# Kernel tuning notes

Hardware: AMD Instinct MI355X
Metric: run time of the kernel (lower is better)

Reference implementation:

```python
import jax, jax.numpy as jnp
import numpy as np

N = 100000
E = 1600000
IN_CH = 128
OUT_CH = 128
NUM_REL = 16
NUM_BASES = 8


def setup_inputs() -> dict:
    key = jax.random.key(0)
    k1, k2, k3, k4, k5, k6 = jax.random.split(key, 6)
    x = jax.random.normal(k1, (N, IN_CH), dtype=jnp.float32)
    edge_index = jax.random.randint(k2, (2, E), 0, N, dtype=jnp.int64)
    edge_type = jax.random.randint(k3, (E,), 0, NUM_REL, dtype=jnp.int64)
    # glorot-style init for basis weights (last slot = root weight) and comp
    wscale = np.sqrt(6.0 / (IN_CH + OUT_CH)).astype(np.float32)
    weight = jax.random.uniform(k4, (NUM_BASES + 1, IN_CH, OUT_CH), dtype=jnp.float32,
                                minval=-wscale, maxval=wscale)
    cscale = np.sqrt(6.0 / (NUM_REL + NUM_BASES)).astype(np.float32)
    comp = jax.random.uniform(k5, (NUM_REL, NUM_BASES), dtype=jnp.float32,
                              minval=-cscale, maxval=cscale)
    bias = jnp.zeros((OUT_CH,), dtype=jnp.float32)
    return {"x": x, "weight": weight, "comp": comp, "bias": bias,
            "edge_index": edge_index, "edge_type": edge_type, "num_nodes": N}


def reference(x, weight, comp, bias, edge_index, edge_type, num_nodes):
    """RGCN with basis decomposition, mean aggregation, root weight + bias.

    agg[i, b, :] = (1/deg(i)) * sum_{e: dst(e)=i} comp[etype(e), b] * x[src(e)]
    out = concat_b(agg, x_root) @ weight.reshape(-1, out_ch) + bias
    """
    src = edge_index[0]
    dst = edge_index[1]
    num_bases = comp.shape[1]
    coeff = comp[edge_type]            # [E, B] per-edge basis coefficients
    msg = x[src]                       # [E, in] gathered neighbor features
    # per-basis scatter-add into destination nodes (loop over small fixed B)
    aggs = [jax.ops.segment_sum(msg * coeff[:, b:b + 1], dst, num_segments=num_nodes)
            for b in range(num_bases)]
    agg = jnp.stack(aggs, axis=1)      # [N, B, in]
    # mean normalization by in-degree of destination node
    deg = jax.ops.segment_sum(jnp.ones((src.shape[0],), dtype=x.dtype), dst,
                              num_segments=num_nodes)
    agg = agg / jnp.maximum(deg, 1.0)[:, None, None]
    # [N, (B+1)*in]: bases first, then root features (matches weight layout)
    feat = jnp.concatenate([agg.reshape(num_nodes, -1), x], axis=1)
    out = feat @ weight.reshape(-1, weight.shape[-1]) + bias
    return out
```

## Files before the change

### kernel.cpp

```cpp
#include <hip/hip_runtime.h>
#include <hip/hip_bf16.h>
#include <stdint.h>


#define FPAD 1160
#define SCAT_CH 8192

typedef __attribute__((ext_vector_type(8))) __bf16 bf16x8;
typedef __attribute__((ext_vector_type(4))) float f32x4;
typedef __attribute__((ext_vector_type(2))) float f32x2;

#define RFL(v) __builtin_amdgcn_readfirstlane(v)

__global__ __launch_bounds__(256) void k_prep(const float* __restrict__ x,
                                              __hip_bfloat16* __restrict__ xb,
                                              uint8_t* __restrict__ xq, int n4,
                                              const float* __restrict__ W,
                                              __hip_bfloat16* __restrict__ Wf,
                                              const int* __restrict__ dst, int E,
                                              int* __restrict__ bcnt, int NB,
                                              int xbB, int wpB, int hbB) {
    extern __shared__ int sc[];
    int b = blockIdx.x;
    if (b < xbB) {
        int i = b * 256 + threadIdx.x;
        if (i < n4) {
            float4 v = ((const float4*)x)[i];
            __hip_bfloat16 h0 = __float2bfloat16(v.x), h1 = __float2bfloat16(v.y);
            __hip_bfloat16 h2 = __float2bfloat16(v.z), h3 = __float2bfloat16(v.w);
            uint32_t p0 = ((uint32_t)*(uint16_t*)&h1 << 16) | *(uint16_t*)&h0;
            uint32_t p1 = ((uint32_t)*(uint16_t*)&h3 << 16) | *(uint16_t*)&h2;
            ((uint2*)xb)[i] = make_uint2(p0, p1);
            uint32_t q = __builtin_amdgcn_cvt_pk_fp8_f32(v.x, v.y, 0u, 0);
            q = __builtin_amdgcn_cvt_pk_fp8_f32(v.z, v.w, q, 1);
            ((uint32_t*)xq)[i] = q;
        }
    } else if (b < xbB + wpB) {
        int idx = (b - xbB) * 256 + threadIdx.x;
        if (idx < 1152 * 128) {
            int k = idx >> 7, n = idx & 127;
            int kb = k >> 5, hi = (k >> 3) & 3, j = k & 7;
            Wf[((((kb << 2) + hi) << 7 | n) << 3) | j] = __float2bfloat16(W[idx]);
        }
    } else {
        for (int i = threadIdx.x; i < NB; i += 256) sc[i] = 0;
        __syncthreads();
        int hb = b - xbB - wpB;
        int stride = hbB * 256;
        for (int e = hb * 256 + threadIdx.x; e < E; e += stride)
            atomicAdd(&sc[dst[e] >> 7], 1);
        __syncthreads();
        for (int i = threadIdx.x; i < NB; i += 256) {
            int c = sc[i];
            if (c) atomicAdd(&bcnt[i], c);
        }
    }
}

__global__ __launch_bounds__(1024) void k_bscan(const int* __restrict__ bcnt, int NB,
                                                int E, int N,
                                                int* __restrict__ base,
                                                int* __restrict__ cursor,
                                                int* __restrict__ row_ptr,
                                                int* __restrict__ csr) {
    __shared__ int s[1024];
    int t = threadIdx.x;
    int v = (t < NB) ? bcnt[t] : 0;
    s[t] = v;
    __syncthreads();
    for (int off = 1; off < 1024; off <<= 1) {
        int u = (t >= off) ? s[t - off] : 0;
        __syncthreads();
        s[t] += u;
        __syncthreads();
    }
    int excl = (t > 0) ? s[t - 1] : 0;
    if (t < NB) { base[t] = excl; cursor[t] = excl; }
    if (t == 0) { base[NB] = E; row_ptr[N] = E; }
    if (t < 24) csr[E + t] = 0;
}

__global__ __launch_bounds__(256) void k_bscatter(const int* __restrict__ src,
                                                  const int* __restrict__ dst,
                                                  const int* __restrict__ et,
                                                  int E, int NB,
                                                  int* __restrict__ cursor,
                                                  int* __restrict__ brec) {
    extern __shared__ int sm[];
    int* cnt = sm;
    int* gb  = sm + NB;
    for (int i = threadIdx.x; i < NB; i += 256) cnt[i] = 0;
    __syncthreads();
    int e0 = blockIdx.x * SCAT_CH;
    int e1 = min(e0 + SCAT_CH, E);
    for (int e = e0 + threadIdx.x; e < e1; e += 256)
        atomicAdd(&cnt[dst[e] >> 7], 1);
    __syncthreads();
    for (int i = threadIdx.x; i < NB; i += 256) {
        int c = cnt[i];
        gb[i] = c ? atomicAdd(&cursor[i], c) : 0;
    }
    __syncthreads();
    for (int i = threadIdx.x; i < NB; i += 256) cnt[i] = 0;
    __syncthreads();
    for (int e = e0 + threadIdx.x; e < e1; e += 256) {
        int d = dst[e];
        int bk = d >> 7;
        int off = atomicAdd(&cnt[bk], 1);
        brec[gb[bk] + off] = (src[e] << 11) | ((d & 127) << 4) | (et[e] & 15);
    }
}

__global__ __launch_bounds__(256) void k_bsort(const int* __restrict__ brec,
                                               const int* __restrict__ base,
                                               int N,
                                               int* __restrict__ row_ptr,
                                               int* __restrict__ csr) {
    __shared__ int cnt[128], st[128];
    int b = blockIdx.x;
    int s0 = base[b], s1 = base[b + 1];
    int t = threadIdx.x;
    if (t < 128) cnt[t] = 0;
    __syncthreads();
    for (int i = s0 + t; i < s1; i += 256)
        atomicAdd(&cnt[(brec[i] >> 4) & 127], 1);
    __syncthreads();
    if (t < 128) st[t] = cnt[t];
    __syncthreads();
    for (int off = 1; off < 128; off <<= 1) {
        int u = 0;
        if (t < 128 && t >= off) u = st[t - off];
        __syncthreads();
        if (t < 128) st[t] += u;
        __syncthreads();
    }
    if (t < 128) {
        int excl = st[t] - cnt[t];
        int d = b * 128 + t;
        if (d < N) row_ptr[d] = s0 + excl;
        cnt[t] = excl;
    }
    __syncthreads();
    for (int i = s0 + t; i < s1; i += 256) {
        int r = brec[i];
        int d7 = (r >> 4) & 127;
        int off = atomicAdd(&cnt[d7], 1);
        csr[s0 + off] = ((r >> 11) << 4) | (r & 15);
    }
}

#define GATH(pp) ((uint32_t)xq16[(uint32_t)((pp) >> 4) * 64u + (uint32_t)lane])

#define CONS1(pp, raw) do {                                               \
    uint32_t _r = (raw);                                                  \
    float _x0 = __builtin_amdgcn_cvt_f32_fp8(_r, 0);                      \
    float _x1 = __builtin_amdgcn_cvt_f32_fp8(_r, 1);                      \
    const f32x2* _cf = (const f32x2*)(comp + ((pp) & 15) * 8);            \
    f32x2 _xx0 = (f32x2){_x0, _x0};                                       \
    f32x2 _xx1 = (f32x2){_x1, _x1};                                       \
    f32x2 _c0 = _cf[0], _c1 = _cf[1], _c2 = _cf[2], _c3 = _cf[3];         \
    a0[0] += _c0 * _xx0; a0[1] += _c1 * _xx0;                             \
    a0[2] += _c2 * _xx0; a0[3] += _c3 * _xx0;                             \
    a1[0] += _c0 * _xx1; a1[1] += _c1 * _xx1;                             \
    a1[2] += _c2 * _xx1; a1[3] += _c3 * _xx1;                             \
} while (0)

__global__ __launch_bounds__(512, 8) void k_fused(const uint8_t* __restrict__ xq,
                                                  const __hip_bfloat16* __restrict__ xb,
                                                  const float* __restrict__ comp,
                                                  const int* __restrict__ row_ptr,
                                                  const int* __restrict__ csr,
                                                  const __hip_bfloat16* __restrict__ Wf,
                                                  const float* __restrict__ bias,
                                                  float* __restrict__ out, int M) {
    __shared__ __hip_bfloat16 fl[16][FPAD];
    __shared__ int snext;
    const uint16_t* __restrict__ xq16 = (const uint16_t*)xq;
    const uint32_t* __restrict__ xb32 = (const uint32_t*)xb;
    int t = threadIdx.x;
    int wid = t >> 6, lane = t & 63;
    int i0 = blockIdx.x * 16;
    if (t == 0) snext = 0;
    __syncthreads();

    #pragma unroll 1
    while (true) {
        int grab = 0;
        if (lane == 0) grab = atomicAdd(&snext, 1);
        int lr = RFL(__shfl(grab, 0));
        if (lr >= 16) break;
        int iu = i0 + lr;
        f32x2 a0[4], a1[4];
        #pragma unroll
        for (int b = 0; b < 4; b++) { a0[b] = (f32x2){0.f, 0.f}; a1[b] = (f32x2){0.f, 0.f}; }
        int s0 = 0, s1 = 0;
        if (iu < M) {
            s0 = RFL(row_ptr[iu]);
            s1 = RFL(row_ptr[iu + 1]);
        }

        int jj = s0;
        int p0 = RFL(csr[jj]),     p1 = RFL(csr[jj + 1]);
        int p2 = RFL(csr[jj + 2]), p3 = RFL(csr[jj + 3]);
        int p4 = RFL(csr[jj + 4]), p5 = RFL(csr[jj + 5]);
        int p6 = RFL(csr[jj + 6]), p7 = RFL(csr[jj + 7]);
        uint32_t w0 = GATH(p0), w1 = GATH(p1), w2 = GATH(p2), w3 = GATH(p3);
        uint32_t w4 = GATH(p4), w5 = GATH(p5), w6 = GATH(p6), w7 = GATH(p7);
        int q0 = RFL(csr[jj + 8]),  q1 = RFL(csr[jj + 9]);
        int q2 = RFL(csr[jj + 10]), q3 = RFL(csr[jj + 11]);
        int q4 = RFL(csr[jj + 12]), q5 = RFL(csr[jj + 13]);
        int q6 = RFL(csr[jj + 14]), q7 = RFL(csr[jj + 15]);
        uint32_t v0 = GATH(q0), v1 = GATH(q1), v2 = GATH(q2), v3 = GATH(q3);
        uint32_t v4 = GATH(q4), v5 = GATH(q5), v6 = GATH(q6), v7 = GATH(q7);

        #pragma unroll 1
        while (jj + 16 < s1) {
            int r0 = RFL(csr[jj + 16]), r1 = RFL(csr[jj + 17]);
            int r2 = RFL(csr[jj + 18]), r3 = RFL(csr[jj + 19]);
            int r4 = RFL(csr[jj + 20]), r5 = RFL(csr[jj + 21]);
            int r6 = RFL(csr[jj + 22]), r7 = RFL(csr[jj + 23]);
            uint32_t u0 = GATH(r0), u1 = GATH(r1), u2 = GATH(r2), u3 = GATH(r3);
            uint32_t u4 = GATH(r4), u5 = GATH(r5), u6 = GATH(r6), u7 = GATH(r7);
            CONS1(p0, w0); CONS1(p1, w1); CONS1(p2, w2); CONS1(p3, w3);
            CONS1(p4, w4); CONS1(p5, w5); CONS1(p6, w6); CONS1(p7, w7);
            p0 = q0; p1 = q1; p2 = q2; p3 = q3;
            p4 = q4; p5 = q5; p6 = q6; p7 = q7;
            w0 = v0; w1 = v1; w2 = v2; w3 = v3;
            w4 = v4; w5 = v5; w6 = v6; w7 = v7;
            q0 = r0; q1 = r1; q2 = r2; q3 = r3;
            q4 = r4; q5 = r5; q6 = r6; q7 = r7;
            v0 = u0; v1 = u1; v2 = u2; v3 = u3;
            v4 = u4; v5 = u5; v6 = u6; v7 = u7;
            jj += 8;
        }
        CONS1(p0, (jj + 0 < s1) ? w0 : 0u);
        CONS1(p1, (jj + 1 < s1) ? w1 : 0u);
        CONS1(p2, (jj + 2 < s1) ? w2 : 0u);
        CONS1(p3, (jj + 3 < s1) ? w3 : 0u);
        CONS1(p4, (jj + 4 < s1) ? w4 : 0u);
        CONS1(p5, (jj + 5 < s1) ? w5 : 0u);
        CONS1(p6, (jj + 6 < s1) ? w6 : 0u);
        CONS1(p7, (jj + 7 < s1) ? w7 : 0u);
        CONS1(q0, (jj + 8 < s1) ? v0 : 0u);
        CONS1(q1, (jj + 9 < s1) ? v1 : 0u);
        CONS1(q2, (jj + 10 < s1) ? v2 : 0u);
        CONS1(q3, (jj + 11 < s1) ? v3 : 0u);
        CONS1(q4, (jj + 12 < s1) ? v4 : 0u);
        CONS1(q5, (jj + 13 < s1) ? v5 : 0u);
        CONS1(q6, (jj + 14 < s1) ? v6 : 0u);
        CONS1(q7, (jj + 15 < s1) ? v7 : 0u);

        float inv = 1.0f / fmaxf((float)(s1 - s0), 1.0f);
        #pragma unroll
        for (int b = 0; b < 8; b++) {
            __hip_bfloat16 h0 = __float2bfloat16(a0[b >> 1][b & 1] * inv);
            __hip_bfloat16 h1 = __float2bfloat16(a1[b >> 1][b & 1] * inv);
            uint32_t pk = ((uint32_t)*(uint16_t*)&h1 << 16) | *(uint16_t*)&h0;
            *(uint32_t*)&fl[lr][b * 128 + lane * 2] = pk;
        }
        uint32_t rr = (iu < M) ? xb32[(uint32_t)iu * 64u + lane] : 0u;
        *(uint32_t*)&fl[lr][1024 + lane * 2] = rr;
    }

    int lo = lane & 15, hi = lane >> 4;
    int wcol = wid * 16 + lo;
    const bf16x8* wv = (const bf16x8*)Wf;
    bf16x8 bA = wv[(hi << 7) + wcol];
    bf16x8 bB = wv[(((1 << 2) + hi) << 7) + wcol];
    float bs = bias[wcol];
    __syncthreads();

    f32x4 acc = (f32x4){0.f, 0.f, 0.f, 0.f};
    bf16x8 aA = *(const bf16x8*)&fl[lo][hi * 8];
    bf16x8 aB = *(const bf16x8*)&fl[lo][32 + hi * 8];
    #pragma unroll 4
    for (int kb = 0; kb < 34; kb++) {
        bf16x8 aN = *(const bf16x8*)&fl[lo][(kb + 2) * 32 + hi * 8];
        bf16x8 bN = wv[((((kb + 2) << 2) + hi) << 7) + wcol];
        acc = __builtin_amdgcn_mfma_f32_16x16x32_bf16(aA, bA, acc, 0, 0, 0);
        aA = aB; bA = bB; aB = aN; bB = bN;
    }
    acc = __builtin_amdgcn_mfma_f32_16x16x32_bf16(aA, bA, acc, 0, 0, 0);
    acc = __builtin_amdgcn_mfma_f32_16x16x32_bf16(aB, bB, acc, 0, 0, 0);

    #pragma unroll
    for (int q = 0; q < 4; q++) {
        int row = i0 + hi * 4 + q;
        if (row < M)
            out[(size_t)row * 128 + wcol] = acc[q] + bs;
    }
}

extern "C" void kernel_launch(void* const* d_in, const int* in_sizes, int n_in,
                              void* d_out, int out_size, void* d_ws, size_t ws_size,
                              hipStream_t stream) {
    const float* x      = (const float*)d_in[0];
    const float* weight = (const float*)d_in[1];
    const float* comp   = (const float*)d_in[2];
    const float* bias   = (const float*)d_in[3];
    const int*   eidx   = (const int*)d_in[4];
    const int*   etype  = (const int*)d_in[5];

    int N = in_sizes[0] / 128;
    int E = in_sizes[5];
    const int* srcA = eidx;
    const int* dstA = eidx + E;
    int NB = (N + 127) >> 7;

    uint8_t* ws = (uint8_t*)d_ws;
    size_t off = 0;
    auto take = [&](size_t bytes) -> void* {
        void* p = ws + off;
        off = (off + bytes + 255) & ~(size_t)255;
        return p;
    };
    __hip_bfloat16* xb = (__hip_bfloat16*)take((size_t)N * 128 * sizeof(__hip_bfloat16));
    uint8_t* xq        = (uint8_t*)take((size_t)N * 128);
    __hip_bfloat16* Wf = (__hip_bfloat16*)take((size_t)1152 * 128 * sizeof(__hip_bfloat16));
    int* row_ptr = (int*)take((size_t)(N + 1) * sizeof(int));
    int* bcnt    = (int*)take((size_t)NB * sizeof(int));
    int* base    = (int*)take((size_t)(NB + 1) * sizeof(int));
    int* cursor  = (int*)take((size_t)NB * sizeof(int));
    int* brec    = (int*)take((size_t)E * sizeof(int));
    int* csr     = (int*)take((size_t)(E + 24) * sizeof(int));
    (void)ws_size;

    int n4 = N * 128 / 4;
    int xbB = (n4 + 255) / 256;
    int wpB = (1152 * 128 + 255) / 256;
    int hbB = 256;
    int scB = (E + SCAT_CH - 1) / SCAT_CH;

    hipMemsetAsync(bcnt, 0, (size_t)NB * sizeof(int), stream);
    k_prep<<<xbB + wpB + hbB, 256, NB * sizeof(int), stream>>>(
        x, xb, xq, n4, weight, Wf, dstA, E, bcnt, NB, xbB, wpB, hbB);
    k_bscan<<<1, 1024, 0, stream>>>(bcnt, NB, E, N, base, cursor, row_ptr, csr);
    k_bscatter<<<scB, 256, 2 * NB * sizeof(int), stream>>>(
        srcA, dstA, etype, E, NB, cursor, brec);
    k_bsort<<<NB, 256, 0, stream>>>(brec, base, N, row_ptr, csr);
    k_fused<<<(N + 15) / 16, 512, 0, stream>>>(xq, xb, comp, row_ptr, csr, Wf, bias,
                                               (float*)d_out, N);
}
```

Baseline: 187.9 us.

## Pad per-node CSR segments to multiples of eight with zero-coefficient sentinel

Each destination node's edge list in the CSR is padded up to a multiple of 8, and the padding slots are filled with a sentinel whose relation index points at a zeroed coefficient row (comp17 row 16). The gather loop can then drop the per-element bounds selects in its tail and skip the second half of the tail when it is not needed. Row start and degree are stored as separate arrays. The cost is a larger CSR buffer, an extra fill pass over it in the sort kernel, and wasted gathers on the padding slots.

```diff
diff --git a/kernel.cpp b/kernel.cpp
--- a/kernel.cpp
+++ b/kernel.cpp
@@ -5,6 +5,7 @@
 
 #define FPAD 1160
 #define SCAT_CH 8192
+#define PADV 16
 
 typedef __attribute__((ext_vector_type(8))) __bf16 bf16x8;
 typedef __attribute__((ext_vector_type(4))) float f32x4;
@@ -58,11 +59,12 @@
 }
 
 __global__ __launch_bounds__(1024) void k_bscan(const int* __restrict__ bcnt, int NB,
-                                                int E, int N,
+                                                int E,
                                                 int* __restrict__ base,
                                                 int* __restrict__ cursor,
-                                                int* __restrict__ row_ptr,
-                                                int* __restrict__ csr) {
+                                                const float* __restrict__ comp,
+                                                float* __restrict__ comp17,
+                                                int* __restrict__ csr, int csrTot) {
     __shared__ int s[1024];
     int t = threadIdx.x;
     int v = (t < NB) ? bcnt[t] : 0;
@@ -76,8 +78,9 @@
     }
     int excl = (t > 0) ? s[t - 1] : 0;
     if (t < NB) { base[t] = excl; cursor[t] = excl; }
-    if (t == 0) { base[NB] = E; row_ptr[N] = E; }
-    if (t < 24) csr[E + t] = 0;
+    if (t == 0) base[NB] = E;
+    if (t < 136) comp17[t] = (t < 128) ? comp[t] : 0.f;
+    if (t >= 136 && t < 160) csr[csrTot + (t - 136)] = PADV;
 }
 
 __global__ __launch_bounds__(256) void k_bscatter(const int* __restrict__ src,
@@ -114,18 +117,21 @@
 __global__ __launch_bounds__(256) void k_bsort(const int* __restrict__ brec,
                                                const int* __restrict__ base,
                                                int N,
-                                               int* __restrict__ row_ptr,
+                                               int* __restrict__ rps,
+                                               int* __restrict__ dga,
                                                int* __restrict__ csr) {
     __shared__ int cnt[128], st[128];
     int b = blockIdx.x;
-    int s0 = base[b], s1 = base[b + 1];
+    int s0g = base[b], s1g = base[b + 1];
+    int raw = s1g - s0g;
+    int pbase = s0g + b * 1024;
     int t = threadIdx.x;
     if (t < 128) cnt[t] = 0;
     __syncthreads();
-    for (int i = s0 + t; i < s1; i += 256)
+    for (int i = s0g + t; i < s1g; i += 256)
         atomicAdd(&cnt[(brec[i] >> 4) & 127], 1);
     __syncthreads();
-    if (t < 128) st[t] = cnt[t];
+    if (t < 128) st[t] = (cnt[t] + 7) & ~7;
     __syncthreads();
     for (int off = 1; off < 128; off <<= 1) {
         int u = 0;
@@ -135,27 +141,28 @@
         __syncthreads();
     }
     if (t < 128) {
-        int excl = st[t] - cnt[t];
+        int pexcl = st[t] - ((cnt[t] + 7) & ~7);
         int d = b * 128 + t;
-        if (d < N) row_ptr[d] = s0 + excl;
-        cnt[t] = excl;
-    }
-    __syncthreads();
-    for (int i = s0 + t; i < s1; i += 256) {
+        if (d < N) { rps[d] = pbase + pexcl; dga[d] = cnt[t]; }
+        cnt[t] = pexcl;
+    }
+    for (int i = t; i < raw + 1024; i += 256) csr[pbase + i] = PADV;
+    __syncthreads();
+    for (int i = s0g + t; i < s1g; i += 256) {
         int r = brec[i];
         int d7 = (r >> 4) & 127;
         int off = atomicAdd(&cnt[d7], 1);
-        csr[s0 + off] = ((r >> 11) << 4) | (r & 15);
-    }
-}
-
-#define GATH(pp) ((uint32_t)xq16[(uint32_t)((pp) >> 4) * 64u + (uint32_t)lane])
+        csr[pbase + off] = ((r >> 11) << 5) | (r & 15);
+    }
+}
+
+#define GATH(pp) ((uint32_t)xq16[(uint32_t)((pp) >> 5) * 64u + (uint32_t)lane])
 
 #define CONS1(pp, raw) do {                                               \
     uint32_t _r = (raw);                                                  \
     float _x0 = __builtin_amdgcn_cvt_f32_fp8(_r, 0);                      \
     float _x1 = __builtin_amdgcn_cvt_f32_fp8(_r, 1);                      \
-    const f32x2* _cf = (const f32x2*)(comp + ((pp) & 15) * 8);            \
+    const f32x2* _cf = (const f32x2*)(comp17 + ((pp) & 31) * 8);          \
     f32x2 _xx0 = (f32x2){_x0, _x0};                                       \
     f32x2 _xx1 = (f32x2){_x1, _x1};                                       \
     f32x2 _c0 = _cf[0], _c1 = _cf[1], _c2 = _cf[2], _c3 = _cf[3];         \
@@ -167,8 +174,9 @@
 
 __global__ __launch_bounds__(512, 8) void k_fused(const uint8_t* __restrict__ xq,
                                                   const __hip_bfloat16* __restrict__ xb,
-                                                  const float* __restrict__ comp,
-                                                  const int* __restrict__ row_ptr,
+                                                  const float* __restrict__ comp17,
+                                                  const int* __restrict__ rps,
+                                                  const int* __restrict__ dga,
                                                   const int* __restrict__ csr,
                                                   const __hip_bfloat16* __restrict__ Wf,
                                                   const float* __restrict__ bias,
@@ -193,64 +201,58 @@
         f32x2 a0[4], a1[4];
         #pragma unroll
         for (int b = 0; b < 4; b++) { a0[b] = (f32x2){0.f, 0.f}; a1[b] = (f32x2){0.f, 0.f}; }
-        int s0 = 0, s1 = 0;
+        int s0 = 0, dg = 0;
         if (iu < M) {
-            s0 = RFL(row_ptr[iu]);
-            s1 = RFL(row_ptr[iu + 1]);
-        }
-
-        int jj = s0;
-        int p0 = RFL(csr[jj]),     p1 = RFL(csr[jj + 1]);
-        int p2 = RFL(csr[jj + 2]), p3 = RFL(csr[jj + 3]);
-        int p4 = RFL(csr[jj + 4]), p5 = RFL(csr[jj + 5]);
-        int p6 = RFL(csr[jj + 6]), p7 = RFL(csr[jj + 7]);
-        uint32_t w0 = GATH(p0), w1 = GATH(p1), w2 = GATH(p2), w3 = GATH(p3);
-        uint32_t w4 = GATH(p4), w5 = GATH(p5), w6 = GATH(p6), w7 = GATH(p7);
-        int q0 = RFL(csr[jj + 8]),  q1 = RFL(csr[jj + 9]);
-        int q2 = RFL(csr[jj + 10]), q3 = RFL(csr[jj + 11]);
-        int q4 = RFL(csr[jj + 12]), q5 = RFL(csr[jj + 13]);
-        int q6 = RFL(csr[jj + 14]), q7 = RFL(csr[jj + 15]);
-        uint32_t v0 = GATH(q0), v1 = GATH(q1), v2 = GATH(q2), v3 = GATH(q3);
-        uint32_t v4 = GATH(q4), v5 = GATH(q5), v6 = GATH(q6), v7 = GATH(q7);
-
-        #pragma unroll 1
-        while (jj + 16 < s1) {
-            int r0 = RFL(csr[jj + 16]), r1 = RFL(csr[jj + 17]);
-            int r2 = RFL(csr[jj + 18]), r3 = RFL(csr[jj + 19]);
-            int r4 = RFL(csr[jj + 20]), r5 = RFL(csr[jj + 21]);
-            int r6 = RFL(csr[jj + 22]), r7 = RFL(csr[jj + 23]);
-            uint32_t u0 = GATH(r0), u1 = GATH(r1), u2 = GATH(r2), u3 = GATH(r3);
-            uint32_t u4 = GATH(r4), u5 = GATH(r5), u6 = GATH(r6), u7 = GATH(r7);
+            s0 = RFL(rps[iu]);
+            dg = RFL(dga[iu]);
+        }
+
+        if (dg > 0) {
+            int plen = (dg + 7) & ~7;
+            int s1 = s0 + plen;
+            int jj = s0;
+            int p0 = RFL(csr[jj]),     p1 = RFL(csr[jj + 1]);
+            int p2 = RFL(csr[jj + 2]), p3 = RFL(csr[jj + 3]);
+            int p4 = RFL(csr[jj + 4]), p5 = RFL(csr[jj + 5]);
+            int p6 = RFL(csr[jj + 6]), p7 = RFL(csr[jj + 7]);
+            uint32_t w0 = GATH(p0), w1 = GATH(p1), w2 = GATH(p2), w3 = GATH(p3);
+            uint32_t w4 = GATH(p4), w5 = GATH(p5), w6 = GATH(p6), w7 = GATH(p7);
+            int q0 = RFL(csr[jj + 8]),  q1 = RFL(csr[jj + 9]);
+            int q2 = RFL(csr[jj + 10]), q3 = RFL(csr[jj + 11]);
+            int q4 = RFL(csr[jj + 12]), q5 = RFL(csr[jj + 13]);
+            int q6 = RFL(csr[jj + 14]), q7 = RFL(csr[jj + 15]);
+            uint32_t v0 = GATH(q0), v1 = GATH(q1), v2 = GATH(q2), v3 = GATH(q3);
+            uint32_t v4 = GATH(q4), v5 = GATH(q5), v6 = GATH(q6), v7 = GATH(q7);
+
+            #pragma unroll 1
+            while (jj + 16 < s1) {
+                int r0 = RFL(csr[jj + 16]), r1 = RFL(csr[jj + 17]);
+                int r2 = RFL(csr[jj + 18]), r3 = RFL(csr[jj + 19]);
+                int r4 = RFL(csr[jj + 20]), r5 = RFL(csr[jj + 21]);
+                int r6 = RFL(csr[jj + 22]), r7 = RFL(csr[jj + 23]);
+                uint32_t u0 = GATH(r0), u1 = GATH(r1), u2 = GATH(r2), u3 = GATH(r3);
+                uint32_t u4 = GATH(r4), u5 = GATH(r5), u6 = GATH(r6), u7 = GATH(r7);
+                CONS1(p0, w0); CONS1(p1, w1); CONS1(p2, w2); CONS1(p3, w3);
+                CONS1(p4, w4); CONS1(p5, w5); CONS1(p6, w6); CONS1(p7, w7);
+                p0 = q0; p1 = q1; p2 = q2; p3 = q3;
+                p4 = q4; p5 = q5; p6 = q6; p7 = q7;
+                w0 = v0; w1 = v1; w2 = v2; w3 = v3;
+                w4 = v4; w5 = v5; w6 = v6; w7 = v7;
+                q0 = r0; q1 = r1; q2 = r2; q3 = r3;
+                q4 = r4; q5 = r5; q6 = r6; q7 = r7;
+                v0 = u0; v1 = u1; v2 = u2; v3 = u3;
+                v4 = u4; v5 = u5; v6 = u6; v7 = u7;
+                jj += 8;
+            }
             CONS1(p0, w0); CONS1(p1, w1); CONS1(p2, w2); CONS1(p3, w3);
             CONS1(p4, w4); CONS1(p5, w5); CONS1(p6, w6); CONS1(p7, w7);
-            p0 = q0; p1 = q1; p2 = q2; p3 = q3;
-            p4 = q4; p5 = q5; p6 = q6; p7 = q7;
-            w0 = v0; w1 = v1; w2 = v2; w3 = v3;
-            w4 = v4; w5 = v5; w6 = v6; w7 = v7;
-            q0 = r0; q1 = r1; q2 = r2; q3 = r3;
-            q4 = r4; q5 = r5; q6 = r6; q7 = r7;
-            v0 = u0; v1 = u1; v2 = u2; v3 = u3;
-            v4 = u4; v5 = u5; v6 = u6; v7 = u7;
-            jj += 8;
-        }
-        CONS1(p0, (jj + 0 < s1) ? w0 : 0u);
-        CONS1(p1, (jj + 1 < s1) ? w1 : 0u);
-        CONS1(p2, (jj + 2 < s1) ? w2 : 0u);
-        CONS1(p3, (jj + 3 < s1) ? w3 : 0u);
-        CONS1(p4, (jj + 4 < s1) ? w4 : 0u);
-        CONS1(p5, (jj + 5 < s1) ? w5 : 0u);
-        CONS1(p6, (jj + 6 < s1) ? w6 : 0u);
-        CONS1(p7, (jj + 7 < s1) ? w7 : 0u);
-        CONS1(q0, (jj + 8 < s1) ? v0 : 0u);
-        CONS1(q1, (jj + 9 < s1) ? v1 : 0u);
-        CONS1(q2, (jj + 10 < s1) ? v2 : 0u);
-        CONS1(q3, (jj + 11 < s1) ? v3 : 0u);
-        CONS1(q4, (jj + 12 < s1) ? v4 : 0u);
-        CONS1(q5, (jj + 13 < s1) ? v5 : 0u);
-        CONS1(q6, (jj + 14 < s1) ? v6 : 0u);
-        CONS1(q7, (jj + 15 < s1) ? v7 : 0u);
-
-        float inv = 1.0f / fmaxf((float)(s1 - s0), 1.0f);
+            if (jj + 8 < s1) {
+                CONS1(q0, v0); CONS1(q1, v1); CONS1(q2, v2); CONS1(q3, v3);
+                CONS1(q4, v4); CONS1(q5, v5); CONS1(q6, v6); CONS1(q7, v7);
+            }
+        }
+
+        float inv = 1.0f / fmaxf((float)dg, 1.0f);
         #pragma unroll
         for (int b = 0; b < 8; b++) {
             __hip_bfloat16 h0 = __float2bfloat16(a0[b >> 1][b & 1] * inv);
@@ -306,6 +308,7 @@
     const int* srcA = eidx;
     const int* dstA = eidx + E;
     int NB = (N + 127) >> 7;
+    int csrTot = E + NB * 1024;
 
     uint8_t* ws = (uint8_t*)d_ws;
     size_t off = 0;
@@ -317,12 +320,14 @@
     __hip_bfloat16* xb = (__hip_bfloat16*)take((size_t)N * 128 * sizeof(__hip_bfloat16));
     uint8_t* xq        = (uint8_t*)take((size_t)N * 128);
     __hip_bfloat16* Wf = (__hip_bfloat16*)take((size_t)1152 * 128 * sizeof(__hip_bfloat16));
-    int* row_ptr = (int*)take((size_t)(N + 1) * sizeof(int));
+    float* comp17 = (float*)take(136 * sizeof(float));
+    int* rps     = (int*)take((size_t)N * sizeof(int));
+    int* dga     = (int*)take((size_t)N * sizeof(int));
     int* bcnt    = (int*)take((size_t)NB * sizeof(int));
     int* base    = (int*)take((size_t)(NB + 1) * sizeof(int));
     int* cursor  = (int*)take((size_t)NB * sizeof(int));
     int* brec    = (int*)take((size_t)E * sizeof(int));
-    int* csr     = (int*)take((size_t)(E + 24) * sizeof(int));
+    int* csr     = (int*)take((size_t)(csrTot + 24) * sizeof(int));
     (void)ws_size;
 
     int n4 = N * 128 / 4;
@@ -334,10 +339,11 @@
     hipMemsetAsync(bcnt, 0, (size_t)NB * sizeof(int), stream);
     k_prep<<<xbB + wpB + hbB, 256, NB * sizeof(int), stream>>>(
         x, xb, xq, n4, weight, Wf, dstA, E, bcnt, NB, xbB, wpB, hbB);
-    k_bscan<<<1, 1024, 0, stream>>>(bcnt, NB, E, N, base, cursor, row_ptr, csr);
+    k_bscan<<<1, 1024, 0, stream>>>(bcnt, NB, E, base, cursor, comp, comp17,
+                                    csr, csrTot);
     k_bscatter<<<scB, 256, 2 * NB * sizeof(int), stream>>>(
         srcA, dstA, etype, E, NB, cursor, brec);
-    k_bsort<<<NB, 256, 0, stream>>>(brec, base, N, row_ptr, csr);
-    k_fused<<<(N + 15) / 16, 512, 0, stream>>>(xq, xb, comp, row_ptr, csr, Wf, bias,
-                                               (float*)d_out, N);
-}
+    k_bsort<<<NB, 256, 0, stream>>>(brec, base, N, rps, dga, csr);
+    k_fused<<<(N + 15) / 16, 512, 0, stream>>>(xq, xb, comp17, rps, dga, csr,
+                                               Wf, bias, (float*)d_out, N);
+}
```

After: 189.3 us. Within noise of the previous version (+0.7%).
